# Performance work log

Measured on AMD Instinct MI355X. Metric: run time of the kernel, lower is better.

The kernel has to match this reference:

```python
import jax, jax.numpy as jnp
import numpy as np

T, H, I, E, TOPK = 8192, 2048, 4096, 8, 2

def setup_inputs() -> dict:
    key = jax.random.key(0)
    k1, k2, k3, k4 = jax.random.split(key, 4)
    x = jax.random.normal(k1, (T, H), dtype=jnp.float32)
    gate_w = jax.random.normal(k2, (E, H), dtype=jnp.float32) * 0.02
    ws = jax.random.normal(k3, (E, 2 * I, H), dtype=jnp.float32) * 0.02
    w2s = jax.random.normal(k4, (E, H, I), dtype=jnp.float32) * 0.02
    return {"x": x, "gate_w": gate_w, "ws": ws, "w2s": w2s, "top_k": TOPK}

def reference(x, gate_w, ws, w2s, top_k):
    num_tokens = x.shape[0]
    num_experts = ws.shape[0]
    inter = w2s.shape[2]
    # --- router (fused_topk): softmax -> top-k -> renormalize ---
    logits = x @ gate_w.T                       # [T, E]
    probs = jax.nn.softmax(logits, axis=-1)
    topk_w, topk_ids = jax.lax.top_k(probs, top_k)   # [T, K]
    if top_k > 1:
        topk_w = topk_w / jnp.sum(topk_w, axis=-1, keepdims=True)
    # dense combine-weights [E, T]: sum of routing weights per (token, expert)
    tok = jnp.arange(num_tokens)
    cw = jnp.zeros((num_tokens, num_experts), dtype=x.dtype)
    cw = cw.at[tok[:, None], topk_ids].add(topk_w)
    cw = cw.T                                   # [E, T]
    # --- fused_experts: per-expert gated-SiLU MLP, weighted combine ---
    def body(acc, inp):
        e_ws, e_w2, e_cw = inp                  # [2I,H], [H,I], [T]
        gu = x @ e_ws.T                         # [T, 2I]
        g, u = gu[:, :inter], gu[:, inter:]
        h = jax.nn.silu(g) * u                  # SiluAndMul
        out = h @ e_w2.T                        # [T, H]
        return acc + e_cw[:, None] * out, None
    init = jnp.zeros_like(x)
    final, _ = jax.lax.scan(body, init, (ws, w2s, cw))
    return final
```

## Files before the change

### kernel.cpp

```cpp
#include <hip/hip_runtime.h>
#include <hip/hip_fp16.h>
#include <cstdint>
#include <cstddef>

#define TTOK 8192
#define HD   2048
#define ID   4096
#define NE   8
#define NPAIR (TTOK * 2)
#define PADROWS 18432
#define RBMAX 72

typedef _Float16 h8 __attribute__((ext_vector_type(8)));
typedef float    f4 __attribute__((ext_vector_type(4)));

#define VMWAIT(n) asm volatile("s_waitcnt vmcnt(" #n ")" ::: "memory")
#define MEMFENCE  asm volatile("" ::: "memory")
#define BAR()     __builtin_amdgcn_s_barrier()

__device__ __forceinline__ void async_cp16(const void* g, void* l) {
  __builtin_amdgcn_global_load_lds(
      (const __attribute__((address_space(1))) unsigned int*)g,
      (__attribute__((address_space(3))) unsigned int*)l, 16, 0, 0);
}

__device__ __forceinline__ f4 zero4() { f4 z = {0.f, 0.f, 0.f, 0.f}; return z; }

template <bool NT>
__global__ void cvt_kernel(const float* __restrict__ src, _Float16* __restrict__ dst, size_t n) {
  size_t stride = (size_t)gridDim.x * blockDim.x * 8;
  for (size_t i = ((size_t)blockIdx.x * blockDim.x + threadIdx.x) * 8; i < n; i += stride) {
    const float4* s = (const float4*)(src + i);
    float4 a = s[0], b = s[1];
    h8 o;
    o[0] = (_Float16)a.x; o[1] = (_Float16)a.y; o[2] = (_Float16)a.z; o[3] = (_Float16)a.w;
    o[4] = (_Float16)b.x; o[5] = (_Float16)b.y; o[6] = (_Float16)b.z; o[7] = (_Float16)b.w;
    if constexpr (NT) __builtin_nontemporal_store(o, (h8*)(dst + i));
    else *(h8*)(dst + i) = o;
  }
}

__device__ __forceinline__ void cvt_w2_half(const float* __restrict__ w2f,
                                            _Float16* __restrict__ dst,
                                            int kh, int cb, int ncb) {
  const size_t n = (size_t)NE * HD * 2048;
  size_t stride = (size_t)ncb * 512 * 8;
  for (size_t j = ((size_t)cb * 512 + threadIdx.x) * 8; j < n; j += stride) {
    size_t row = j >> 11, ic = j & 2047;
    const float4* s = (const float4*)(w2f + row * ID + (size_t)kh * 2048 + ic);
    float4 a = s[0], b = s[1];
    h8 o;
    o[0] = (_Float16)a.x; o[1] = (_Float16)a.y; o[2] = (_Float16)a.z; o[3] = (_Float16)a.w;
    o[4] = (_Float16)b.x; o[5] = (_Float16)b.y; o[6] = (_Float16)b.z; o[7] = (_Float16)b.w;
    *(h8*)(dst + row * 2048 + ic) = o;
  }
}

__global__ __launch_bounds__(256) void gate_kernel(
    const float* __restrict__ x, const float* __restrict__ gw,
    int* __restrict__ counts, int* __restrict__ tids, float* __restrict__ tw) {
  int lane = threadIdx.x & 63;
  int t = blockIdx.x * 4 + (threadIdx.x >> 6);
  const float* xr = x + (size_t)t * HD;
  float acc[NE];
#pragma unroll
  for (int e = 0; e < NE; e++) acc[e] = 0.f;
  for (int j = lane; j < HD; j += 64) {
    float xv = xr[j];
#pragma unroll
    for (int e = 0; e < NE; e++) acc[e] += xv * gw[e * HD + j];
  }
#pragma unroll
  for (int off = 32; off > 0; off >>= 1) {
#pragma unroll
    for (int e = 0; e < NE; e++) acc[e] += __shfl_xor(acc[e], off, 64);
  }
  if (lane == 0) {
    int e0 = 0; float v0 = acc[0];
#pragma unroll
    for (int e = 1; e < NE; e++) if (acc[e] > v0) { v0 = acc[e]; e0 = e; }
    int e1 = -1; float v1 = -1e30f;
#pragma unroll
    for (int e = 0; e < NE; e++) if (e != e0 && acc[e] > v1) { v1 = acc[e]; e1 = e; }
    float b = __expf(v1 - v0);
    float w0 = 1.f / (1.f + b);
    tids[2 * t] = e0; tids[2 * t + 1] = e1;
    tw[2 * t] = w0;   tw[2 * t + 1] = b * w0;
    atomicAdd(&counts[e0], 1); atomicAdd(&counts[e1], 1);
  }
}

__global__ void scan_kernel(const int* __restrict__ counts, int* __restrict__ offs,
                            int* __restrict__ cursor) {
  if (threadIdx.x == 0 && blockIdx.x == 0) {
    int off = 0;
    for (int e = 0; e < NE; e++) {
      offs[e] = off; cursor[e] = off;
      off += ((counts[e] + 255) >> 8) << 8;
    }
    offs[NE] = off;
  }
}

__global__ void scatter_kernel(const int* __restrict__ tids, const float* __restrict__ tw,
                               int* __restrict__ cursor, int* __restrict__ perm,
                               float* __restrict__ pw, int* __restrict__ pairpos) {
  int t = blockIdx.x * 256 + threadIdx.x;
#pragma unroll
  for (int k = 0; k < 2; k++) {
    int e = tids[2 * t + k];
    int pos = atomicAdd(&cursor[e], 1);
    perm[pos] = t; pw[pos] = tw[2 * t + k];
    pairpos[2 * t + k] = pos;
  }
}

__global__ void padfill_kernel(const int* __restrict__ counts, const int* __restrict__ offs,
                               int* __restrict__ perm) {
  int s = blockIdx.x * 256 + threadIdx.x;
#pragma unroll
  for (int e = 0; e < NE; e++) {
    if (s >= offs[e] + counts[e] && s < offs[e + 1]) perm[s] = -1;
  }
}

#define LA(BB, H) ((BB) * 65536 + (H) * 16384)
#define LB(BB, H) ((BB) * 65536 + 32768 + (H) * 16384)
#define RD(boff) (*(const h8*)(smem + (boff)))

#define LOAD_AF(BB, MH) do { \
  af[0][0] = RD(LA(BB,MH) + amoff + 0*2048 + sa0); \
  af[0][1] = RD(LA(BB,MH) + amoff + 0*2048 + sa1); \
  af[1][0] = RD(LA(BB,MH) + amoff + 1*2048 + sa0); \
  af[1][1] = RD(LA(BB,MH) + amoff + 1*2048 + sa1); \
  af[2][0] = RD(LA(BB,MH) + amoff + 2*2048 + sa0); \
  af[2][1] = RD(LA(BB,MH) + amoff + 2*2048 + sa1); \
  af[3][0] = RD(LA(BB,MH) + amoff + 3*2048 + sa0); \
  af[3][1] = RD(LA(BB,MH) + amoff + 3*2048 + sa1); } while (0)

#define LOAD_BFG(BB) do { \
  bfg[0][0] = RD(LB(BB,0) + bnoff + 0*2048 + sa0); \
  bfg[0][1] = RD(LB(BB,0) + bnoff + 0*2048 + sa1); \
  bfg[1][0] = RD(LB(BB,0) + bnoff + 1*2048 + sa0); \
  bfg[1][1] = RD(LB(BB,0) + bnoff + 1*2048 + sa1); } while (0)

#define LOAD_BFU(BB) do { \
  bfu[0][0] = RD(LB(BB,1) + bnoff + 0*2048 + sa0); \
  bfu[0][1] = RD(LB(BB,1) + bnoff + 0*2048 + sa1); \
  bfu[1][0] = RD(LB(BB,1) + bnoff + 1*2048 + sa0); \
  bfu[1][1] = RD(LB(BB,1) + bnoff + 1*2048 + sa1); } while (0)

#define MM(MH,NH,BF,M,N) \
  acc[MH][NH][M][N] = __builtin_amdgcn_mfma_f32_16x16x32_f16(af[M][0], BF[N][0], acc[MH][NH][M][N], 0, 0, 0); \
  acc[MH][NH][M][N] = __builtin_amdgcn_mfma_f32_16x16x32_f16(af[M][1], BF[N][1], acc[MH][NH][M][N], 0, 0, 0);

#define MFMAQ(MH,NH,BF) do { __builtin_amdgcn_s_setprio(1); \
  MM(MH,NH,BF,0,0) MM(MH,NH,BF,0,1) MM(MH,NH,BF,1,0) MM(MH,NH,BF,1,1) \
  MM(MH,NH,BF,2,0) MM(MH,NH,BF,2,1) MM(MH,NH,BF,3,0) MM(MH,NH,BF,3,1) \
  __builtin_amdgcn_s_setprio(0); } while (0)

#define STG(gp, ldsbyte, kt) do { \
  async_cp16(gp[0] + (size_t)(kt) * 64, smem + (ldsbyte) + (wid * 2 + 0) * 1024 + lane * 16); \
  async_cp16(gp[1] + (size_t)(kt) * 64, smem + (ldsbyte) + (wid * 2 + 1) * 1024 + lane * 16); } while (0)

#define ACC_ZERO() do { \
  _Pragma("unroll") for (int mh = 0; mh < 2; mh++) \
  _Pragma("unroll") for (int nh = 0; nh < 2; nh++) \
  _Pragma("unroll") for (int m = 0; m < 4; m++) \
  _Pragma("unroll") for (int n = 0; n < 2; n++) acc[mh][nh][m][n] = zero4(); } while (0)

#define KLOOP(NI) \
  STG(gA[0], LA(0,0), 0); STG(gA[1], LA(0,1), 0); \
  STG(gB[0], LB(0,0), 0); STG(gB[1], LB(0,1), 0); \
  STG(gA[0], LA(1,0), 1); STG(gB[1], LB(1,1), 1); \
  VMWAIT(4); \
  BAR(); \
  for (int i = 0; i < (NI); ++i) { \
    bool last = (i == (NI) - 1); \
    int kt1 = 2 * i + 1, kt2 = 2 * i + 2, kt3 = 2 * i + 3; \
     \
    MEMFENCE; LOAD_AF(0,0); LOAD_BFG(0); \
    STG(gA[1], LA(1,1), kt1); STG(gB[0], LB(1,0), kt1); \
    BAR(); MEMFENCE; MFMAQ(0,0,bfg); BAR(); \
     \
    MEMFENCE; LOAD_BFU(0); \
    BAR(); MEMFENCE; MFMAQ(0,1,bfu); BAR(); \
     \
    MEMFENCE; LOAD_AF(0,1); \
    if (!last) STG(gA[0], LA(0,0), kt2); \
    BAR(); MEMFENCE; MFMAQ(1,1,bfu); BAR(); \
     \
    MEMFENCE; \
    if (!last) { STG(gB[1], LB(0,1), kt2); VMWAIT(4); } else { VMWAIT(0); } \
    BAR(); MEMFENCE; MFMAQ(1,0,bfg); BAR(); \
     \
    MEMFENCE; LOAD_AF(1,0); LOAD_BFG(1); \
    if (!last) { STG(gA[1], LA(0,1), kt2); STG(gB[0], LB(0,0), kt2); } \
    BAR(); MEMFENCE; MFMAQ(0,0,bfg); BAR(); \
     \
    MEMFENCE; LOAD_BFU(1); \
    BAR(); MEMFENCE; MFMAQ(0,1,bfu); BAR(); \
     \
    MEMFENCE; LOAD_AF(1,1); \
    if (!last) STG(gA[0], LA(1,0), kt3); \
    BAR(); MEMFENCE; MFMAQ(1,1,bfu); BAR(); \
     \
    MEMFENCE; \
    if (!last) { STG(gB[1], LB(1,1), kt3); VMWAIT(4); } \
    BAR(); MEMFENCE; MFMAQ(1,0,bfg); BAR(); \
  }

__device__ __forceinline__ int expert_of(const int* offs, int row0) {
  int e = 0;
#pragma unroll
  for (int k = 1; k < NE; k++) if (offs[k] <= row0) e = k;
  return e;
}

__global__ __launch_bounds__(512, 2) void gemm1_kernel(
    const _Float16* __restrict__ xh, const _Float16* __restrict__ wsh,
    const int* __restrict__ offs, const int* __restrict__ perm,
    _Float16* __restrict__ hb,
    const float* __restrict__ w2f, _Float16* __restrict__ w2h0) {
  int bx = blockIdx.x, gyy = blockIdx.y;
  if (gyy >= RBMAX) {
    cvt_w2_half(w2f, w2h0, 0, (gyy - RBMAX) * 32 + bx, 256);
    return;
  }
  int row0 = gyy << 8;
  if (row0 >= offs[NE]) return;
  int e = expert_of(offs, row0);
  int n0 = bx << 7;

  __shared__ char smem[131072];
  int tid = threadIdx.x, lane = tid & 63, wid = tid >> 6;
  int wm = wid >> 2, wn = wid & 3;
  int lr = lane & 15, ks = lane >> 4;
  int sa0 = lr * 128 + (((ks)     ^ (lr & 7)) << 4);
  int sa1 = lr * 128 + (((ks + 4) ^ (lr & 7)) << 4);
  int amoff = wm * 8192;
  int bnoff = wn * 4096;

  int srow = wid * 16 + (lane >> 3);
  int scol = ((lane & 7) ^ (lane >> 3)) * 8;
  const _Float16* gA[2][2]; const _Float16* gB[2][2];
#pragma unroll
  for (int h = 0; h < 2; h++)
#pragma unroll
    for (int j = 0; j < 2; j++) {
      int r = row0 + h * 128 + srow + j * 8;
      int pv = perm[r]; if (pv < 0) pv = 0;
      gA[h][j] = xh + (size_t)pv * HD + scol;
      gB[h][j] = wsh + ((size_t)e * 2 * ID + (size_t)h * ID + n0 + srow + j * 8) * HD + scol;
    }

  f4 acc[2][2][4][2];
  h8 af[4][2], bfg[2][2], bfu[2][2];
  ACC_ZERO();

  KLOOP(16)

#pragma unroll
  for (int mh = 0; mh < 2; mh++)
#pragma unroll
    for (int m = 0; m < 4; m++)
#pragma unroll
      for (int n = 0; n < 2; n++)
#pragma unroll
        for (int r = 0; r < 4; r++) {
          float g = acc[mh][0][m][n][r], u = acc[mh][1][m][n][r];
          float hv = g / (1.f + __expf(-g)) * u;
          int row = row0 + mh * 128 + wm * 64 + m * 16 + ks * 4 + r;
          int col = n0 + wn * 32 + n * 16 + lr;
          __builtin_nontemporal_store((_Float16)hv, hb + (size_t)row * ID + col);
        }
}

__global__ __launch_bounds__(512, 2) void gemm2_kernel(
    const _Float16* __restrict__ hb, const _Float16* __restrict__ w2hk,
    const int* __restrict__ offs, _Float16* __restrict__ hb2k, int kh,
    const float* __restrict__ w2f, _Float16* __restrict__ w2h_other) {
  int bx = blockIdx.x, gyy = blockIdx.y;
  if (gyy >= RBMAX) {
    cvt_w2_half(w2f, w2h_other, 1, (gyy - RBMAX) * 8 + bx, 64);
    return;
  }
  int row0 = gyy << 8;
  if (row0 >= offs[NE]) return;
  int e = expert_of(offs, row0);
  int n0 = bx << 8;
  size_t k0 = (size_t)kh * 2048;

  __shared__ char smem[131072];
  int tid = threadIdx.x, lane = tid & 63, wid = tid >> 6;
  int wm = wid >> 2, wn = wid & 3;
  int lr = lane & 15, ks = lane >> 4;
  int sa0 = lr * 128 + (((ks)     ^ (lr & 7)) << 4);
  int sa1 = lr * 128 + (((ks + 4) ^ (lr & 7)) << 4);
  int amoff = wm * 8192;
  int bnoff = wn * 4096;

  int srow = wid * 16 + (lane >> 3);
  int scol = ((lane & 7) ^ (lane >> 3)) * 8;
  const _Float16* gA[2][2]; const _Float16* gB[2][2];
#pragma unroll
  for (int h = 0; h < 2; h++)
#pragma unroll
    for (int j = 0; j < 2; j++) {
      gA[h][j] = hb + ((size_t)(row0 + h * 128 + srow + j * 8)) * ID + k0 + scol;
      gB[h][j] = w2hk + ((size_t)e * HD + n0 + h * 128 + srow + j * 8) * 2048 + scol;
    }

  f4 acc[2][2][4][2];
  h8 af[4][2], bfg[2][2], bfu[2][2];
  ACC_ZERO();

  KLOOP(16)

#pragma unroll
  for (int mh = 0; mh < 2; mh++)
#pragma unroll
    for (int nh = 0; nh < 2; nh++)
#pragma unroll
      for (int m = 0; m < 4; m++)
#pragma unroll
        for (int n = 0; n < 2; n++)
#pragma unroll
          for (int r = 0; r < 4; r++) {
            int row = row0 + mh * 128 + wm * 64 + m * 16 + ks * 4 + r;
            int col = n0 + nh * 128 + wn * 32 + n * 16 + lr;
            hb2k[(size_t)row * HD + col] = (_Float16)acc[mh][nh][m][n][r];
          }
}

__global__ __launch_bounds__(256) void combine_kernel(
    const _Float16* __restrict__ hb2, const int* __restrict__ pairpos,
    const float* __restrict__ pw, float* __restrict__ out) {
  int i = blockIdx.x * 256 + threadIdx.x;
  int t = i >> 8, g = (i & 255) * 8;
  int p0 = pairpos[2 * t], p1 = pairpos[2 * t + 1];
  float w0 = pw[p0], w1 = pw[p1];
  const _Float16* hb2b = hb2 + (size_t)PADROWS * HD;
  h8 a0 = *(const h8*)(hb2  + (size_t)p0 * HD + g);
  h8 a1 = *(const h8*)(hb2b + (size_t)p0 * HD + g);
  h8 b0 = *(const h8*)(hb2  + (size_t)p1 * HD + g);
  h8 b1 = *(const h8*)(hb2b + (size_t)p1 * HD + g);
  f4 o0, o1;
#pragma unroll
  for (int j = 0; j < 4; j++)
    o0[j] = w0 * ((float)a0[j] + (float)a1[j]) + w1 * ((float)b0[j] + (float)b1[j]);
#pragma unroll
  for (int j = 0; j < 4; j++)
    o1[j] = w0 * ((float)a0[j + 4] + (float)a1[j + 4]) + w1 * ((float)b0[j + 4] + (float)b1[j + 4]);
  __builtin_nontemporal_store(o0, (f4*)(out + (size_t)t * HD + g));
  __builtin_nontemporal_store(o1, (f4*)(out + (size_t)t * HD + g + 4));
}

extern "C" void kernel_launch(void* const* d_in, const int* in_sizes, int n_in,
                              void* d_out, int out_size, void* d_ws, size_t ws_size,
                              hipStream_t stream) {
  const float* x   = (const float*)d_in[0];
  const float* gw  = (const float*)d_in[1];
  const float* wsf = (const float*)d_in[2];
  const float* w2f = (const float*)d_in[3];

  int* counts   = (int*)d_ws;
  int* offs     = counts + 8;
  int* cursor   = offs + 16;
  int* tids     = cursor + 8;
  float* tw     = (float*)(tids + NPAIR);
  int* perm     = (int*)(tw + NPAIR);
  float* pw     = (float*)(perm + PADROWS);
  int* pairpos  = (int*)(pw + PADROWS);

  char* base = (char*)d_ws;
  size_t off_xh   = (size_t)512 * 1024;
  size_t off_hb   = off_xh + (size_t)TTOK * HD * 2;
  size_t off_w2h0 = off_hb + (size_t)PADROWS * ID * 2;
  size_t off_big  = off_w2h0 + (size_t)NE * HD * 2048 * 2;
  size_t need     = off_big + (size_t)NE * 2 * ID * HD * 2;
  if (ws_size < need) return;

  _Float16* xh   = (_Float16*)(base + off_xh);
  _Float16* hb   = (_Float16*)(base + off_hb);
  _Float16* w2h0 = (_Float16*)(base + off_w2h0);
  _Float16* wsh  = (_Float16*)(base + off_big);
  _Float16* w2h1 = (_Float16*)(base + off_big);
  _Float16* hb2  = (_Float16*)(base + off_big + (size_t)NE * HD * 2048 * 2);

  hipMemsetAsync(counts, 0, 64, stream);

  cvt_kernel<false><<<2048, 256, 0, stream>>>(x, xh, (size_t)TTOK * HD);
  cvt_kernel<true><<<4096, 256, 0, stream>>>(wsf, wsh, (size_t)NE * 2 * ID * HD);
  gate_kernel<<<TTOK / 4, 256, 0, stream>>>(x, gw, counts, tids, tw);
  scan_kernel<<<1, 64, 0, stream>>>(counts, offs, cursor);
  scatter_kernel<<<TTOK / 256, 256, 0, stream>>>(tids, tw, cursor, perm, pw, pairpos);
  padfill_kernel<<<PADROWS / 256, 256, 0, stream>>>(counts, offs, perm);

  gemm1_kernel<<<dim3(ID / 128, RBMAX + 8), 512, 0, stream>>>(
      xh, wsh, offs, perm, hb, w2f, w2h0);

  gemm2_kernel<<<dim3(HD / 256, RBMAX + 8), 512, 0, stream>>>(
      hb, w2h0, offs, hb2, 0, w2f, w2h1);

  gemm2_kernel<<<dim3(HD / 256, RBMAX), 512, 0, stream>>>(
      hb, w2h1, offs, hb2 + (size_t)PADROWS * HD, 1, w2f, (_Float16*)nullptr);

  combine_kernel<<<(TTOK * HD / 8) / 256, 256, 0, stream>>>(
      hb2, pairpos, pw, (float*)d_out);
}
```

Measured before the change: 1.439 ms.

## Halve barriers in gemm1 K-loop and fuse x fp16 conversion into gate

```diff
diff --git a/kernel.cpp b/kernel.cpp
--- a/kernel.cpp
+++ b/kernel.cpp
@@ -58,15 +58,18 @@
 
 __global__ __launch_bounds__(256) void gate_kernel(
     const float* __restrict__ x, const float* __restrict__ gw,
-    int* __restrict__ counts, int* __restrict__ tids, float* __restrict__ tw) {
+    int* __restrict__ counts, int* __restrict__ tids, float* __restrict__ tw,
+    _Float16* __restrict__ xh) {
   int lane = threadIdx.x & 63;
   int t = blockIdx.x * 4 + (threadIdx.x >> 6);
   const float* xr = x + (size_t)t * HD;
+  _Float16* xhr = xh + (size_t)t * HD;
   float acc[NE];
 #pragma unroll
   for (int e = 0; e < NE; e++) acc[e] = 0.f;
   for (int j = lane; j < HD; j += 64) {
     float xv = xr[j];
+    xhr[j] = (_Float16)xv;
 #pragma unroll
     for (int e = 0; e < NE; e++) acc[e] += xv * gw[e * HD + j];
   }
@@ -179,35 +182,22 @@
     bool last = (i == (NI) - 1); \
     int kt1 = 2 * i + 1, kt2 = 2 * i + 2, kt3 = 2 * i + 3; \
      \
-    MEMFENCE; LOAD_AF(0,0); LOAD_BFG(0); \
+    MEMFENCE; LOAD_AF(0,0); LOAD_BFG(0); LOAD_BFU(0); \
     STG(gA[1], LA(1,1), kt1); STG(gB[0], LB(1,0), kt1); \
-    BAR(); MEMFENCE; MFMAQ(0,0,bfg); BAR(); \
-     \
-    MEMFENCE; LOAD_BFU(0); \
-    BAR(); MEMFENCE; MFMAQ(0,1,bfu); BAR(); \
+    BAR(); MEMFENCE; MFMAQ(0,0,bfg); MFMAQ(0,1,bfu); BAR(); \
      \
     MEMFENCE; LOAD_AF(0,1); \
-    if (!last) STG(gA[0], LA(0,0), kt2); \
-    BAR(); MEMFENCE; MFMAQ(1,1,bfu); BAR(); \
+    if (!last) { STG(gA[0], LA(0,0), kt2); STG(gB[1], LB(0,1), kt2); VMWAIT(4); } \
+    else { VMWAIT(0); } \
+    BAR(); MEMFENCE; MFMAQ(1,1,bfu); MFMAQ(1,0,bfg); BAR(); \
      \
-    MEMFENCE; \
-    if (!last) { STG(gB[1], LB(0,1), kt2); VMWAIT(4); } else { VMWAIT(0); } \
-    BAR(); MEMFENCE; MFMAQ(1,0,bfg); BAR(); \
-     \
-    MEMFENCE; LOAD_AF(1,0); LOAD_BFG(1); \
+    MEMFENCE; LOAD_AF(1,0); LOAD_BFG(1); LOAD_BFU(1); \
     if (!last) { STG(gA[1], LA(0,1), kt2); STG(gB[0], LB(0,0), kt2); } \
-    BAR(); MEMFENCE; MFMAQ(0,0,bfg); BAR(); \
-     \
-    MEMFENCE; LOAD_BFU(1); \
-    BAR(); MEMFENCE; MFMAQ(0,1,bfu); BAR(); \
+    BAR(); MEMFENCE; MFMAQ(0,0,bfg); MFMAQ(0,1,bfu); BAR(); \
      \
     MEMFENCE; LOAD_AF(1,1); \
-    if (!last) STG(gA[0], LA(1,0), kt3); \
-    BAR(); MEMFENCE; MFMAQ(1,1,bfu); BAR(); \
-     \
-    MEMFENCE; \
-    if (!last) { STG(gB[1], LB(1,1), kt3); VMWAIT(4); } \
-    BAR(); MEMFENCE; MFMAQ(1,0,bfg); BAR(); \
+    if (!last) { STG(gA[0], LA(1,0), kt3); STG(gB[1], LB(1,1), kt3); VMWAIT(4); } \
+    BAR(); MEMFENCE; MFMAQ(1,1,bfu); MFMAQ(1,0,bfg); BAR(); \
   }
 
 __device__ __forceinline__ int expert_of(const int* offs, int row0) {
@@ -390,9 +380,8 @@
 
   hipMemsetAsync(counts, 0, 64, stream);
 
-  cvt_kernel<false><<<2048, 256, 0, stream>>>(x, xh, (size_t)TTOK * HD);
   cvt_kernel<true><<<4096, 256, 0, stream>>>(wsf, wsh, (size_t)NE * 2 * ID * HD);
-  gate_kernel<<<TTOK / 4, 256, 0, stream>>>(x, gw, counts, tids, tw);
+  gate_kernel<<<TTOK / 4, 256, 0, stream>>>(x, gw, counts, tids, tw, xh);
   scan_kernel<<<1, 64, 0, stream>>>(counts, offs, cursor);
   scatter_kernel<<<TTOK / 256, 256, 0, stream>>>(tids, tw, cursor, perm, pw, pairpos);
   padfill_kernel<<<PADROWS / 256, 256, 0, stream>>>(counts, offs, perm);
```

Result: no change. 1.432 ms (-0.5%).

## Fuse MoE combine into gemm2 epilogue via atomics and merge K halves

Applied to the files above, without the earlier changes.

```diff
diff --git a/kernel.cpp b/kernel.cpp
--- a/kernel.cpp
+++ b/kernel.cpp
@@ -56,17 +56,25 @@
   }
 }
 
+__global__ __launch_bounds__(512) void cvt_w2half_kernel(
+    const float* __restrict__ w2f, _Float16* __restrict__ dst, int kh) {
+  cvt_w2_half(w2f, dst, kh, blockIdx.x, gridDim.x);
+}
+
 __global__ __launch_bounds__(256) void gate_kernel(
     const float* __restrict__ x, const float* __restrict__ gw,
-    int* __restrict__ counts, int* __restrict__ tids, float* __restrict__ tw) {
+    int* __restrict__ counts, int* __restrict__ tids, float* __restrict__ tw,
+    _Float16* __restrict__ xh) {
   int lane = threadIdx.x & 63;
   int t = blockIdx.x * 4 + (threadIdx.x >> 6);
   const float* xr = x + (size_t)t * HD;
+  _Float16* xhr = xh + (size_t)t * HD;
   float acc[NE];
 #pragma unroll
   for (int e = 0; e < NE; e++) acc[e] = 0.f;
   for (int j = lane; j < HD; j += 64) {
     float xv = xr[j];
+    xhr[j] = (_Float16)xv;
 #pragma unroll
     for (int e = 0; e < NE; e++) acc[e] += xv * gw[e * HD + j];
   }
@@ -104,14 +112,13 @@
 
 __global__ void scatter_kernel(const int* __restrict__ tids, const float* __restrict__ tw,
                                int* __restrict__ cursor, int* __restrict__ perm,
-                               float* __restrict__ pw, int* __restrict__ pairpos) {
+                               float* __restrict__ pw) {
   int t = blockIdx.x * 256 + threadIdx.x;
 #pragma unroll
   for (int k = 0; k < 2; k++) {
     int e = tids[2 * t + k];
     int pos = atomicAdd(&cursor[e], 1);
     perm[pos] = t; pw[pos] = tw[2 * t + k];
-    pairpos[2 * t + k] = pos;
   }
 }
 
@@ -277,19 +284,15 @@
 }
 
 __global__ __launch_bounds__(512, 2) void gemm2_kernel(
-    const _Float16* __restrict__ hb, const _Float16* __restrict__ w2hk,
-    const int* __restrict__ offs, _Float16* __restrict__ hb2k, int kh,
-    const float* __restrict__ w2f, _Float16* __restrict__ w2h_other) {
+    const _Float16* __restrict__ hb, const _Float16* __restrict__ w2h0,
+    const _Float16* __restrict__ w2h1, const int* __restrict__ offs,
+    const int* __restrict__ perm, const float* __restrict__ pw,
+    float* __restrict__ out) {
   int bx = blockIdx.x, gyy = blockIdx.y;
-  if (gyy >= RBMAX) {
-    cvt_w2_half(w2f, w2h_other, 1, (gyy - RBMAX) * 8 + bx, 64);
-    return;
-  }
   int row0 = gyy << 8;
   if (row0 >= offs[NE]) return;
   int e = expert_of(offs, row0);
   int n0 = bx << 8;
-  size_t k0 = (size_t)kh * 2048;
 
   __shared__ char smem[131072];
   int tid = threadIdx.x, lane = tid & 63, wid = tid >> 6;
@@ -307,8 +310,8 @@
   for (int h = 0; h < 2; h++)
 #pragma unroll
     for (int j = 0; j < 2; j++) {
-      gA[h][j] = hb + ((size_t)(row0 + h * 128 + srow + j * 8)) * ID + k0 + scol;
-      gB[h][j] = w2hk + ((size_t)e * HD + n0 + h * 128 + srow + j * 8) * 2048 + scol;
+      gA[h][j] = hb + ((size_t)(row0 + h * 128 + srow + j * 8)) * ID + scol;
+      gB[h][j] = w2h0 + ((size_t)e * HD + n0 + h * 128 + srow + j * 8) * 2048 + scol;
     }
 
   f4 acc[2][2][4][2];
@@ -318,42 +321,33 @@
   KLOOP(16)
 
 #pragma unroll
+  for (int h = 0; h < 2; h++)
+#pragma unroll
+    for (int j = 0; j < 2; j++) {
+      gA[h][j] += 2048;
+      gB[h][j] = w2h1 + ((size_t)e * HD + n0 + h * 128 + srow + j * 8) * 2048 + scol;
+    }
+
+  KLOOP(16)
+
+#pragma unroll
   for (int mh = 0; mh < 2; mh++)
 #pragma unroll
-    for (int nh = 0; nh < 2; nh++)
-#pragma unroll
-      for (int m = 0; m < 4; m++)
-#pragma unroll
-        for (int n = 0; n < 2; n++)
-#pragma unroll
-          for (int r = 0; r < 4; r++) {
-            int row = row0 + mh * 128 + wm * 64 + m * 16 + ks * 4 + r;
-            int col = n0 + nh * 128 + wn * 32 + n * 16 + lr;
-            hb2k[(size_t)row * HD + col] = (_Float16)acc[mh][nh][m][n][r];
-          }
-}
-
-__global__ __launch_bounds__(256) void combine_kernel(
-    const _Float16* __restrict__ hb2, const int* __restrict__ pairpos,
-    const float* __restrict__ pw, float* __restrict__ out) {
-  int i = blockIdx.x * 256 + threadIdx.x;
-  int t = i >> 8, g = (i & 255) * 8;
-  int p0 = pairpos[2 * t], p1 = pairpos[2 * t + 1];
-  float w0 = pw[p0], w1 = pw[p1];
-  const _Float16* hb2b = hb2 + (size_t)PADROWS * HD;
-  h8 a0 = *(const h8*)(hb2  + (size_t)p0 * HD + g);
-  h8 a1 = *(const h8*)(hb2b + (size_t)p0 * HD + g);
-  h8 b0 = *(const h8*)(hb2  + (size_t)p1 * HD + g);
-  h8 b1 = *(const h8*)(hb2b + (size_t)p1 * HD + g);
-  f4 o0, o1;
-#pragma unroll
-  for (int j = 0; j < 4; j++)
-    o0[j] = w0 * ((float)a0[j] + (float)a1[j]) + w1 * ((float)b0[j] + (float)b1[j]);
-#pragma unroll
-  for (int j = 0; j < 4; j++)
-    o1[j] = w0 * ((float)a0[j + 4] + (float)a1[j + 4]) + w1 * ((float)b0[j + 4] + (float)b1[j + 4]);
-  __builtin_nontemporal_store(o0, (f4*)(out + (size_t)t * HD + g));
-  __builtin_nontemporal_store(o1, (f4*)(out + (size_t)t * HD + g + 4));
+    for (int m = 0; m < 4; m++)
+#pragma unroll
+      for (int r = 0; r < 4; r++) {
+        int row = row0 + mh * 128 + wm * 64 + m * 16 + ks * 4 + r;
+        int t = perm[row];
+        if (t < 0) continue;
+        float w = pw[row];
+        float* orow = out + (size_t)t * HD + n0;
+#pragma unroll
+        for (int nh = 0; nh < 2; nh++)
+#pragma unroll
+          for (int n = 0; n < 2; n++)
+            atomicAdd(orow + nh * 128 + wn * 32 + n * 16 + lr,
+                      w * acc[mh][nh][m][n][r]);
+      }
 }
 
 extern "C" void kernel_launch(void* const* d_in, const int* in_sizes, int n_in,
@@ -371,7 +365,6 @@
   float* tw     = (float*)(tids + NPAIR);
   int* perm     = (int*)(tw + NPAIR);
   float* pw     = (float*)(perm + PADROWS);
-  int* pairpos  = (int*)(pw + PADROWS);
 
   char* base = (char*)d_ws;
   size_t off_xh   = (size_t)512 * 1024;
@@ -386,26 +379,21 @@
   _Float16* w2h0 = (_Float16*)(base + off_w2h0);
   _Float16* wsh  = (_Float16*)(base + off_big);
   _Float16* w2h1 = (_Float16*)(base + off_big);
-  _Float16* hb2  = (_Float16*)(base + off_big + (size_t)NE * HD * 2048 * 2);
 
   hipMemsetAsync(counts, 0, 64, stream);
-
-  cvt_kernel<false><<<2048, 256, 0, stream>>>(x, xh, (size_t)TTOK * HD);
-  cvt_kernel<true><<<4096, 256, 0, stream>>>(wsf, wsh, (size_t)NE * 2 * ID * HD);
-  gate_kernel<<<TTOK / 4, 256, 0, stream>>>(x, gw, counts, tids, tw);
+  hipMemsetAsync(d_out, 0, (size_t)out_size * 4, stream);
+
+  cvt_kernel<false><<<4096, 256, 0, stream>>>(wsf, wsh, (size_t)NE * 2 * ID * HD);
+  gate_kernel<<<TTOK / 4, 256, 0, stream>>>(x, gw, counts, tids, tw, xh);
   scan_kernel<<<1, 64, 0, stream>>>(counts, offs, cursor);
-  scatter_kernel<<<TTOK / 256, 256, 0, stream>>>(tids, tw, cursor, perm, pw, pairpos);
+  scatter_kernel<<<TTOK / 256, 256, 0, stream>>>(tids, tw, cursor, perm, pw);
   padfill_kernel<<<PADROWS / 256, 256, 0, stream>>>(counts, offs, perm);
 
   gemm1_kernel<<<dim3(ID / 128, RBMAX + 8), 512, 0, stream>>>(
       xh, wsh, offs, perm, hb, w2f, w2h0);
 
-  gemm2_kernel<<<dim3(HD / 256, RBMAX + 8), 512, 0, stream>>>(
-      hb, w2h0, offs, hb2, 0, w2f, w2h1);
+  cvt_w2half_kernel<<<512, 512, 0, stream>>>(w2f, w2h1, 1);
 
   gemm2_kernel<<<dim3(HD / 256, RBMAX), 512, 0, stream>>>(
-      hb, w2h1, offs, hb2 + (size_t)PADROWS * HD, 1, w2f, (_Float16*)nullptr);
-
-  combine_kernel<<<(TTOK * HD / 8) / 256, 256, 0, stream>>>(
-      hb2, pairpos, pw, (float*)d_out);
-}
+      hb, w2h0, w2h1, offs, perm, pw, (float*)d_out);
+}
```

After: 1.495 ms. +3.9%, slower.

## Fuse x half-conversion into gate kernel and merge gemm2 K-halves into one launch

Applied to the files above, without the earlier changes.

```diff
diff --git a/kernel.cpp b/kernel.cpp
--- a/kernel.cpp
+++ b/kernel.cpp
@@ -56,17 +56,25 @@
   }
 }
 
+__global__ __launch_bounds__(512) void cvt_w2half_kernel(
+    const float* __restrict__ w2f, _Float16* __restrict__ dst, int kh) {
+  cvt_w2_half(w2f, dst, kh, blockIdx.x, gridDim.x);
+}
+
 __global__ __launch_bounds__(256) void gate_kernel(
     const float* __restrict__ x, const float* __restrict__ gw,
-    int* __restrict__ counts, int* __restrict__ tids, float* __restrict__ tw) {
+    int* __restrict__ counts, int* __restrict__ tids, float* __restrict__ tw,
+    _Float16* __restrict__ xh) {
   int lane = threadIdx.x & 63;
   int t = blockIdx.x * 4 + (threadIdx.x >> 6);
   const float* xr = x + (size_t)t * HD;
+  _Float16* xhr = xh + (size_t)t * HD;
   float acc[NE];
 #pragma unroll
   for (int e = 0; e < NE; e++) acc[e] = 0.f;
   for (int j = lane; j < HD; j += 64) {
     float xv = xr[j];
+    xhr[j] = (_Float16)xv;
 #pragma unroll
     for (int e = 0; e < NE; e++) acc[e] += xv * gw[e * HD + j];
   }
@@ -277,18 +285,16 @@
 }
 
 __global__ __launch_bounds__(512, 2) void gemm2_kernel(
-    const _Float16* __restrict__ hb, const _Float16* __restrict__ w2hk,
-    const int* __restrict__ offs, _Float16* __restrict__ hb2k, int kh,
-    const float* __restrict__ w2f, _Float16* __restrict__ w2h_other) {
+    const _Float16* __restrict__ hb, const _Float16* __restrict__ w2h0,
+    const _Float16* __restrict__ w2h1, const int* __restrict__ offs,
+    _Float16* __restrict__ hb2) {
   int bx = blockIdx.x, gyy = blockIdx.y;
-  if (gyy >= RBMAX) {
-    cvt_w2_half(w2f, w2h_other, 1, (gyy - RBMAX) * 8 + bx, 64);
-    return;
-  }
   int row0 = gyy << 8;
   if (row0 >= offs[NE]) return;
   int e = expert_of(offs, row0);
   int n0 = bx << 8;
+  int kh = blockIdx.z;
+  const _Float16* w2hk = kh ? w2h1 : w2h0;
   size_t k0 = (size_t)kh * 2048;
 
   __shared__ char smem[131072];
@@ -317,6 +323,7 @@
 
   KLOOP(16)
 
+  _Float16* dst = hb2 + (size_t)kh * PADROWS * HD;
 #pragma unroll
   for (int mh = 0; mh < 2; mh++)
 #pragma unroll
@@ -329,7 +336,9 @@
           for (int r = 0; r < 4; r++) {
             int row = row0 + mh * 128 + wm * 64 + m * 16 + ks * 4 + r;
             int col = n0 + nh * 128 + wn * 32 + n * 16 + lr;
-            hb2k[(size_t)row * HD + col] = (_Float16)acc[mh][nh][m][n][r];
+            hb2[(size_t)kh * PADROWS * HD + (size_t)row * HD + col] =
+                (_Float16)acc[mh][nh][m][n][r];
+            (void)dst;
           }
 }
 
@@ -390,9 +399,8 @@
 
   hipMemsetAsync(counts, 0, 64, stream);
 
-  cvt_kernel<false><<<2048, 256, 0, stream>>>(x, xh, (size_t)TTOK * HD);
-  cvt_kernel<true><<<4096, 256, 0, stream>>>(wsf, wsh, (size_t)NE * 2 * ID * HD);
-  gate_kernel<<<TTOK / 4, 256, 0, stream>>>(x, gw, counts, tids, tw);
+  cvt_kernel<false><<<4096, 256, 0, stream>>>(wsf, wsh, (size_t)NE * 2 * ID * HD);
+  gate_kernel<<<TTOK / 4, 256, 0, stream>>>(x, gw, counts, tids, tw, xh);
   scan_kernel<<<1, 64, 0, stream>>>(counts, offs, cursor);
   scatter_kernel<<<TTOK / 256, 256, 0, stream>>>(tids, tw, cursor, perm, pw, pairpos);
   padfill_kernel<<<PADROWS / 256, 256, 0, stream>>>(counts, offs, perm);
@@ -400,11 +408,10 @@
   gemm1_kernel<<<dim3(ID / 128, RBMAX + 8), 512, 0, stream>>>(
       xh, wsh, offs, perm, hb, w2f, w2h0);
 
-  gemm2_kernel<<<dim3(HD / 256, RBMAX + 8), 512, 0, stream>>>(
-      hb, w2h0, offs, hb2, 0, w2f, w2h1);
-
-  gemm2_kernel<<<dim3(HD / 256, RBMAX), 512, 0, stream>>>(
-      hb, w2h1, offs, hb2 + (size_t)PADROWS * HD, 1, w2f, (_Float16*)nullptr);
+  cvt_w2half_kernel<<<512, 512, 0, stream>>>(w2f, w2h1, 1);
+
+  gemm2_kernel<<<dim3(HD / 256, RBMAX, 2), 512, 0, stream>>>(
+      hb, w2h0, w2h1, offs, hb2);
 
   combine_kernel<<<(TTOK * HD / 8) / 256, 256, 0, stream>>>(
       hb2, pairpos, pw, (float*)d_out);
```

After: 1.389 ms. 3.4% less time.
